# Kernel optimization log

Measured on AMD Instinct MI355X. Metric: run time of the kernel, lower is better.

## Reference

```python
import jax, jax.numpy as jnp
import numpy as np
from jax import lax

SPAN = 11
SIG_RGB = 0.1
SIG_XY = 6.0
SIG_DEPTH = 0.2


def _crf_energy(image, depth, yhat, m_dst, span=SPAN):
    """Vectorized equivalent of the 23x23 double loop.

    For offset d=(dx,dy), the torch code pairs t1 pixel u with t2 pixel u-d.
    jnp.roll(x, (dx,dy)) places x[u-d] at position u; a validity mask replaces
    the slicing.  Class-compatibility r = sum_{c1!=c2} p1[c1] p2[c2]
    = (sum p1)(sum p2) - <p1, p2>.
    """
    B, _, H, W = image.shape
    i = jnp.arange(H)
    j = jnp.arange(W)
    offs = np.array([(dx, dy) for dx in range(-span, span + 1) if dx != 0
                     for dy in range(-span, span + 1) if dy != 0], dtype=np.int32)
    offs = jnp.asarray(offs)  # (484, 2)
    s1 = yhat.sum(axis=1)  # (B,H,W), sums of softmax

    def body(carry, off):
        dx, dy = off[0], off[1]
        valid = (((i - dx >= 0) & (i - dx < H))[:, None]
                 & ((j - dy >= 0) & (j - dy < W))[None, :]).astype(image.dtype)  # (H,W)
        roll2 = lambda x: jnp.roll(x, (dx, dy), axis=(2, 3))
        r_img = roll2(image)
        r_yhat = roll2(yhat)
        r_depth = roll2(depth)
        r_dst = roll2(m_dst)
        drgb = (r_img - image) / SIG_RGB
        drgb_sq = (drgb * drgb).sum(axis=1)                       # (B,H,W)
        dind_sq = (dx * dx + dy * dy).astype(image.dtype) / (SIG_XY * SIG_XY)
        dd = (r_depth - depth) / SIG_DEPTH
        dd_sq = (dd * dd).sum(axis=1)                             # (B,H,W)
        kernel = jnp.exp(-0.5 * (drgb_sq + dind_sq)) + jnp.exp(-0.5 * dd_sq)
        m = r_dst[:, 0] * valid                                   # (B,H,W)
        compat = s1 * r_yhat.sum(axis=1) - (yhat * r_yhat).sum(axis=1)
        energy = (kernel * m * compat).sum() / m.sum()
        return carry, energy

    _, energies = lax.scan(body, None, offs)
    K = 2 * span + 1
    grid = jnp.zeros((K, K), dtype=image.dtype).at[offs[:, 0] + span, offs[:, 1] + span].set(energies)
    # result is (B, K, K) with the same scalar broadcast over batch -> mean == grid.mean()
    return grid.mean()


def setup_inputs() -> dict:
    key = jax.random.key(0)
    ks = jax.random.split(key, 6)
    B, C, H, W = 4, 3, 256, 512
    logit = jax.random.normal(ks[0], (B, C, H, W), dtype=jnp.float32)
    target = jax.random.randint(ks[1], (B, H, W), 0, C, dtype=jnp.int64)
    image = jax.random.uniform(ks[2], (B, 3, H, W), dtype=jnp.float32)
    depth = jax.random.uniform(ks[3], (B, 1, H, W), dtype=jnp.float32)
    destination_map = jax.random.uniform(ks[4], (B, 1, H, W), dtype=jnp.float32)
    source_map = jnp.ones((B, 1, H, W), dtype=jnp.float32)
    return {"logit": logit, "target": target, "image": image, "depth": depth,
            "destination_map": destination_map, "source_map": source_map}


def reference(logit, target, image, depth, destination_map, source_map):
    sg = lax.stop_gradient
    yhat = jax.nn.softmax(logit, axis=1)
    # compute_gcrf_new is called on .data (detached) tensors
    L_gcrf = _crf_energy(sg(image), sg(depth), sg(yhat), sg(destination_map))
    # CrossEntropyLoss(reduction='none')
    log_p = jax.nn.log_softmax(logit, axis=1)
    L_ce = -jnp.take_along_axis(log_p, target[:, None, :, :], axis=1)[:, 0]  # (B,H,W)
    dst = destination_map[:, 0]
    l1 = (L_ce * dst).mean()
    l2 = (L_ce * (1.0 - dst)).mean()
    count = sg(destination_map.mean())  # .item() in torch -> constant
    ce_loss = l1 * (1.0 - count) + l2 * count
    return ce_loss, L_gcrf
```

## Files before the change

### kernel.cpp

```cpp
#include <hip/hip_runtime.h>
#include <hip/hip_fp16.h>

#define H 256
#define W 512
#define HW (H*W)
#define NPIXF 524288.0f
#define SPAN 11
#define KK 23
#define NBINS (KK*KK)

#define LOG2E 1.4426950408889634f
#define CEXP  (-0.7213475204444817f)
#define CIND  (CEXP/36.0f)
#define KRGB  8.4932180f
#define KDEP  4.2466090f

#define TX 32
#define TYR 32
#define TROWS 43
#define TCOLS 43
#define TPIX (TROWS*TCOLS)

#define NTILE 512
#define NCRF (NTILE*2)
#define NSTAT 44

typedef _Float16 h2 __attribute__((ext_vector_type(2)));

struct alignas(16) PixV { h2 rg, bd, y01, y2m; };

__device__ __forceinline__ h2 pack2(float a, float b) {
  h2 r; r.x = (_Float16)a; r.y = (_Float16)b; return r;
}

__device__ __forceinline__ float dpp_sum(float x) {
  x += __int_as_float(__builtin_amdgcn_update_dpp(0, __float_as_int(x), 0x111, 0xf, 0xf, true));
  x += __int_as_float(__builtin_amdgcn_update_dpp(0, __float_as_int(x), 0x112, 0xf, 0xf, true));
  x += __int_as_float(__builtin_amdgcn_update_dpp(0, __float_as_int(x), 0x114, 0xf, 0xf, true));
  x += __int_as_float(__builtin_amdgcn_update_dpp(0, __float_as_int(x), 0x118, 0xf, 0xf, true));
  x += __int_as_float(__builtin_amdgcn_update_dpp(0, __float_as_int(x), 0x142, 0xa, 0xf, true));
  x += __int_as_float(__builtin_amdgcn_update_dpp(0, __float_as_int(x), 0x143, 0xc, 0xf, true));
  return x;
}

__device__ __forceinline__ float wave_sum(float x) {
  #pragma unroll
  for (int s = 1; s < 64; s <<= 1) x += __shfl_xor(x, s, 64);
  return x;
}

__device__ __forceinline__ float paircc(const PixV& C, const PixV& N,
                                        h2 nc01, h2 nc2z, float lind) {
  h2 drg = N.rg - C.rg;
  h2 dbd = N.bd - C.bd;
  h2 sq  = dbd*dbd;
  float dbsq = (float)sq.x;
  float ddsq = (float)sq.y;
#if __has_builtin(__builtin_amdgcn_fdot2)
  float q  = __builtin_amdgcn_fdot2(drg, drg, dbsq, false);
  float a1 = lind - q;
  float w1 = __builtin_amdgcn_fdot2(N.y01, nc01, 1.0f, false);
  float w  = __builtin_amdgcn_fdot2(N.y2m, nc2z, w1, false);
#else
  float dr = (float)drg.x, dg = (float)drg.y;
  float a1 = fmaf(-dr, dr, fmaf(-dg, dg, lind - dbsq));
  float ny0 = (float)N.y01.x, ny1 = (float)N.y01.y, ny2 = (float)N.y2m.x;
  float cy0 = (float)C.y01.x, cy1 = (float)C.y01.y, cy2 = (float)C.y2m.x;
  float w  = fmaf(-ny0, cy0, fmaf(-ny1, cy1, fmaf(-ny2, cy2, 1.0f)));
  (void)nc01; (void)nc2z;
#endif
  float kv = __builtin_amdgcn_exp2f(a1) + __builtin_amdgcn_exp2f(-ddsq);
  return kv * w;
}

__global__ __launch_bounds__(256, 4) void crf_kernel(
    const float* __restrict__ logit, const int* __restrict__ target,
    const float* __restrict__ image, const float* __restrict__ depth,
    const float* __restrict__ dst,
    float* __restrict__ g_bins, float* __restrict__ g_ce,
    float* __restrict__ rowBand, float* __restrict__ colBand) {
  __shared__ PixV  tile[TPIX];
  __shared__ float binsS[4][NBINS];
  __shared__ float redS[12];

  int tx = threadIdx.x;
  int bid = blockIdx.x;
  int lane = tx & 63;
  int wv = tx >> 6;

  if (bid >= NCRF) {
    int k = bid - NCRF;
    float s = 0.f;
    if (k < 22) {
      int row = (k < 11) ? k : (234 + k);
      for (int t = tx; t < 2048; t += 256) {
        int b = t >> 9, j = t & 511;
        s += dst[(size_t)b*HW + row*W + j];
      }
    } else {
      int kc = k - 22;
      int col = (kc < 11) ? kc : (490 + kc);
      for (int t = tx; t < 1024; t += 256) {
        int b = t >> 8, i = t & 255;
        s += dst[(size_t)b*HW + i*W + col];
      }
    }
    s = wave_sum(s);
    if (lane == 0) redS[wv] = s;
    __syncthreads();
    if (tx == 0) {
      float tot = redS[0] + redS[1] + redS[2] + redS[3];
      if (k < 22) rowBand[k] = tot; else colBand[k - 22] = tot;
    }
    return;
  }

  int tileId = bid >> 1;
  int half   = bid & 1;
  int bz = tileId >> 7;
  int rem = tileId & 127;
  int i0 = (rem >> 4) * TYR;
  int j0 = (rem & 15) * TX;
  int co = half ? 0 : 11;
  int cbase = j0 - co;

  const float* lg0 = logit + (size_t)bz*3*HW;
  const float* lg1 = lg0 + HW;
  const float* lg2 = lg0 + 2*HW;
  const float* im0 = image + (size_t)bz*3*HW;
  const float* im1 = im0 + HW;
  const float* im2 = im0 + 2*HW;
  const float* dep = depth + (size_t)bz*HW;
  const float* dsb = dst   + (size_t)bz*HW;
  const int*   tgb = target + (size_t)bz*HW;

  for (int s = tx; s < 4*NBINS; s += 256) ((float*)binsS)[s] = 0.f;

  float v0 = 0.f, v1 = 0.f, v2 = 0.f;
  for (int s = tx; s < TPIX; s += 256) {
    int r = s / TCOLS, c = s - r*TCOLS;
    int gi = i0 + r, gj = cbase + c;
    PixV ph;
    if (gi < H && (unsigned)gj < (unsigned)W) {
      int q = gi*W + gj;
      float l0 = lg0[q], l1 = lg1[q], l2 = lg2[q];
      float mx = fmaxf(l0, fmaxf(l1, l2));
      float e0 = __builtin_amdgcn_exp2f((l0-mx)*LOG2E);
      float e1 = __builtin_amdgcn_exp2f((l1-mx)*LOG2E);
      float e2 = __builtin_amdgcn_exp2f((l2-mx)*LOG2E);
      float S = e0+e1+e2;
      float inv = 1.0f/S;
      float m = dsb[q];
      ph.rg  = pack2(im0[q]*KRGB, im1[q]*KRGB);
      ph.bd  = pack2(im2[q]*KRGB, dep[q]*KDEP);
      ph.y01 = pack2(e0*inv, e1*inv);
      ph.y2m = pack2(e2*inv, m);
      if (half == 0 && r < TYR && c >= co && c < co+TX) {
        int t = tgb[q];
        float lt = (t==0) ? l0 : ((t==1) ? l1 : l2);
        float lce = mx + __logf(S) - lt;
        float t0 = lce * m;
        v0 += t0;
        v1 += lce - t0;
        v2 += m;
      }
    } else {
      ph.rg = ph.bd = pack2(1e30f, 1e30f);
      ph.y01 = ph.y2m = pack2(0.f, 0.f);
    }
    tile[s] = ph;
  }
  __syncthreads();

  int txc = tx & 31, ty = tx >> 5;
  int crow = ty*4;
  int cidx = crow*TCOLS + txc + co;
  PixV c0 = tile[cidx];
  PixV c1 = tile[cidx +   TCOLS];
  PixV c2 = tile[cidx + 2*TCOLS];
  PixV c3 = tile[cidx + 3*TCOLS];
  h2 nc01_0 = -c0.y01, nc01_1 = -c1.y01, nc01_2 = -c2.y01, nc01_3 = -c3.y01;
  h2 nc2z_0; nc2z_0.x = -c0.y2m.x; nc2z_0.y = (_Float16)0.f;
  h2 nc2z_1; nc2z_1.x = -c1.y2m.x; nc2z_1.y = (_Float16)0.f;
  h2 nc2z_2; nc2z_2.x = -c2.y2m.x; nc2z_2.y = (_Float16)0.f;
  h2 nc2z_3; nc2z_3.x = -c3.y2m.x; nc2z_3.y = (_Float16)0.f;
  float cm0 = (float)c0.y2m.y;
  float cm1 = (float)c1.y2m.y;
  float cm2 = (float)c2.y2m.y;
  float cm3 = (float)c3.y2m.y;

  int biLo = half * 11;
  #pragma unroll 1
  for (int bi = biLo; bi < biLo + 11; ++bi) {
    int db = bi - ((bi < 11) ? 11 : 10);
    int nb = cidx + db;
    float lb = CIND * (float)(db*db);
    int bb = SPAN*KK + (db + SPAN);
    PixV w0 = tile[nb +   TCOLS];
    PixV w1 = tile[nb + 2*TCOLS];
    PixV w2 = tile[nb + 3*TCOLS];
    float m0 = (float)w0.y2m.y;
    float m1 = (float)w1.y2m.y;
    float m2 = (float)w2.y2m.y;
    #pragma unroll
    for (int a = 1; a <= 11; ++a) {
      PixV w3 = tile[nb + (a+3)*TCOLS];
      float m3 = (float)w3.y2m.y;
      float lind = fmaf((float)(a*a), CIND, lb);
      float cc0 = paircc(c0, w0, nc01_0, nc2z_0, lind);
      float cc1 = paircc(c1, w1, nc01_1, nc2z_1, lind);
      float cc2 = paircc(c2, w2, nc01_2, nc2z_2, lind);
      float cc3 = paircc(c3, w3, nc01_3, nc2z_3, lind);
      float nd = fmaf(cc3, cm3, fmaf(cc2, cm2, fmaf(cc1, cm1, cc0*cm0)));
      float nr = fmaf(cc3, m3,  fmaf(cc2, m2,  fmaf(cc1, m1,  cc0*m0)));
      nd = dpp_sum(nd);
      nr = dpp_sum(nr);
      if (lane == 63) {
        int id = bb + a*KK;
        binsS[wv][id]       = nd;
        binsS[wv][528 - id] = nr;
      }
      w0 = w1; w1 = w2; w2 = w3;
      m0 = m1; m1 = m2; m2 = m3;
    }
  }
  __syncthreads();

  for (int s = tx; s < NBINS; s += 256) {
    float v = (binsS[0][s] + binsS[1][s]) + (binsS[2][s] + binsS[3][s]);
    if (v != 0.f) unsafeAtomicAdd(&g_bins[s], v);
  }
  if (half == 0) {
    v0 = dpp_sum(v0); v1 = dpp_sum(v1); v2 = dpp_sum(v2);
    if (lane == 63) { redS[wv] = v0; redS[4+wv] = v1; redS[8+wv] = v2; }
    __syncthreads();
    if (tx == 0) {
      unsafeAtomicAdd(&g_ce[0], redS[0]+redS[1]+redS[2]+redS[3]);
      unsafeAtomicAdd(&g_ce[1], redS[4]+redS[5]+redS[6]+redS[7]);
      unsafeAtomicAdd(&g_ce[2], redS[8]+redS[9]+redS[10]+redS[11]);
    }
  }
}

__global__ __launch_bounds__(256) void fin_kernel(const float* __restrict__ g_bins,
                                                  const float* __restrict__ g_ce,
                                                  const float* __restrict__ rowBand,
                                                  const float* __restrict__ colBand,
                                                  const float* __restrict__ dst,
                                                  float* __restrict__ out) {
  __shared__ float corner[22][22];
  __shared__ float rowp[22][23];
  __shared__ float P[23][23];
  __shared__ float rb[22], cb[22];
  __shared__ float TopP[12], BotS[12], LeftP[12], RightS[12];
  __shared__ float red[4];
  int tx = threadIdx.x;
  if (tx < 22) { rb[tx] = rowBand[tx]; cb[tx] = colBand[tx]; }
  for (int t = tx; t < 484; t += 256) {
    int ri = t / 22, ci = t - ri*22;
    int row = (ri < 11) ? ri : (234 + ri);
    int col = (ci < 11) ? ci : (490 + ci);
    float s = 0.f;
    #pragma unroll
    for (int b = 0; b < 4; ++b) s += dst[(size_t)b*HW + row*W + col];
    corner[ri][ci] = s;
  }
  __syncthreads();

  if (tx < 22) {
    float p = 0.f; rowp[tx][0] = 0.f;
    for (int j = 0; j < 22; ++j) { p += corner[tx][j]; rowp[tx][j+1] = p; }
  }
  else if (tx == 32) { float p=0.f; TopP[0]=0.f;   for (int k=1;k<12;++k){ p += rb[k-1];  TopP[k]=p; } }
  else if (tx == 33) { float p=0.f; BotS[0]=0.f;   for (int k=1;k<12;++k){ p += rb[22-k]; BotS[k]=p; } }
  else if (tx == 34) { float p=0.f; LeftP[0]=0.f;  for (int k=1;k<12;++k){ p += cb[k-1];  LeftP[k]=p; } }
  else if (tx == 35) { float p=0.f; RightS[0]=0.f; for (int k=1;k<12;++k){ p += cb[22-k]; RightS[k]=p; } }
  __syncthreads();

  if (tx < 23) {
    float p = 0.f; P[0][tx] = 0.f;
    for (int i = 0; i < 22; ++i) { p += rowp[i][tx]; P[i+1][tx] = p; }
  }
  __syncthreads();

  float S = g_ce[2];
  float esum = 0.f;
  for (int od = tx; od < NBINS; od += 256) {
    int dxp = od / KK, dyp = od - dxp*KK;
    int dx = dxp - SPAN, dy = dyp - SPAN;
    if (dx != 0 && dy != 0) {
      int ax = (dx < 0) ? -dx : 0;
      int bx = (dx > 0) ?  dx : 0;
      int ay = (dy < 0) ? -dy : 0;
      int by = (dy > 0) ?  dy : 0;
      float TLv = P[ax][ay];
      float TRv = P[ax][22] - P[ax][22-by];
      float BLv = P[22][ay] - P[22-bx][ay];
      float BRv = P[22][22] - P[22-bx][22] - P[22][22-by] + P[22-bx][22-by];
      float den = S - TopP[ax] - BotS[bx] - LeftP[ay] - RightS[by]
                + TLv + TRv + BLv + BRv;
      esum += g_bins[od] / den;
    }
  }
  esum = wave_sum(esum);
  int lane = tx & 63, wv = tx >> 6;
  if (lane == 0) red[wv] = esum;
  __syncthreads();
  if (tx == 0) {
    float E = (red[0]+red[1]+red[2]+red[3]) / 529.0f;
    float count = S / NPIXF;
    float l1 = g_ce[0] / NPIXF;
    float l2 = g_ce[1] / NPIXF;
    out[0] = l1*(1.0f - count) + l2*count;
    out[1] = E;
  }
}

extern "C" void kernel_launch(void* const* d_in, const int* in_sizes, int n_in,
                              void* d_out, int out_size, void* d_ws, size_t ws_size,
                              hipStream_t stream) {
  const float* logit  = (const float*)d_in[0];
  const int*   target = (const int*)  d_in[1];
  const float* image  = (const float*)d_in[2];
  const float* depth  = (const float*)d_in[3];
  const float* dstm   = (const float*)d_in[4];
  float* out = (float*)d_out;

  float* ws      = (float*)d_ws;
  float* g_bins  = ws;
  float* g_ce    = ws + NBINS;
  float* rowBand = ws + 532;
  float* colBand = ws + 554;

  hipMemsetAsync(ws, 0, 532*sizeof(float), stream);
  crf_kernel<<<NCRF + NSTAT, 256, 0, stream>>>(logit, target, image, depth, dstm,
                                               g_bins, g_ce, rowBand, colBand);
  fin_kernel<<<1, 256, 0, stream>>>(g_bins, g_ce, rowBand, colBand, dstm, out);
}
```

Before: 174.1 us.

## Pack row pairs into fp16x2 lanes and split pair loop by offset parity

Changes the shared tile layout so each 16-byte entry holds two vertically adjacent pixels, each channel stored as a packed fp16 pair. The pair-energy math, including exp2, then runs on packed half2 vectors. The grid is split four ways per tile, by column half and by parity of the row offset, so each block handles even or odd vertical offsets. The aim is to roughly halve the ALU and exp instruction count per pair and to raise block count. The cost is more duplicated tile loading and softmax work across blocks, plus lower precision in the exponent and weight math, now done fully in fp16.

```diff
diff --git a/kernel.cpp b/kernel.cpp
--- a/kernel.cpp
+++ b/kernel.cpp
@@ -19,18 +19,43 @@
 #define TYR 32
 #define TROWS 43
 #define TCOLS 43
-#define TPIX (TROWS*TCOLS)
+#define NP 22
 
 #define NTILE 512
-#define NCRF (NTILE*2)
+#define NCRF (NTILE*4)
 #define NSTAT 44
 
 typedef _Float16 h2 __attribute__((ext_vector_type(2)));
 
-struct alignas(16) PixV { h2 rg, bd, y01, y2m; };
+struct alignas(16) Pk1 { h2 rr, gg, bb, dd; };
+struct alignas(16) Pk2 { h2 y0, y1, y2, mm; };
 
 __device__ __forceinline__ h2 pack2(float a, float b) {
   h2 r; r.x = (_Float16)a; r.y = (_Float16)b; return r;
+}
+
+__device__ __forceinline__ h2 exp2pk(h2 x) {
+  __half2 hx = __builtin_bit_cast(__half2, x);
+  __half2 hr = h2exp2(hx);
+  return __builtin_bit_cast(h2, hr);
+}
+
+__device__ __forceinline__ h2 alignh(h2 a, h2 b) { h2 r; r.x = a.y; r.y = b.x; return r; }
+__device__ __forceinline__ Pk1 alignP1(const Pk1& a, const Pk1& b) {
+  Pk1 r; r.rr = alignh(a.rr,b.rr); r.gg = alignh(a.gg,b.gg);
+  r.bb = alignh(a.bb,b.bb); r.dd = alignh(a.dd,b.dd); return r;
+}
+__device__ __forceinline__ Pk2 alignP2(const Pk2& a, const Pk2& b) {
+  Pk2 r; r.y0 = alignh(a.y0,b.y0); r.y1 = alignh(a.y1,b.y1);
+  r.y2 = alignh(a.y2,b.y2); r.mm = alignh(a.mm,b.mm); return r;
+}
+
+__device__ __forceinline__ float fdot2f(h2 a, h2 b, float c) {
+#if __has_builtin(__builtin_amdgcn_fdot2)
+  return __builtin_amdgcn_fdot2(a, b, c, false);
+#else
+  return c + (float)a.x*(float)b.x + (float)a.y*(float)b.y;
+#endif
 }
 
 __device__ __forceinline__ float dpp_sum(float x) {
@@ -49,28 +74,76 @@
   return x;
 }
 
-__device__ __forceinline__ float paircc(const PixV& C, const PixV& N,
-                                        h2 nc01, h2 nc2z, float lind) {
-  h2 drg = N.rg - C.rg;
-  h2 dbd = N.bd - C.bd;
-  h2 sq  = dbd*dbd;
-  float dbsq = (float)sq.x;
-  float ddsq = (float)sq.y;
-#if __has_builtin(__builtin_amdgcn_fdot2)
-  float q  = __builtin_amdgcn_fdot2(drg, drg, dbsq, false);
-  float a1 = lind - q;
-  float w1 = __builtin_amdgcn_fdot2(N.y01, nc01, 1.0f, false);
-  float w  = __builtin_amdgcn_fdot2(N.y2m, nc2z, w1, false);
-#else
-  float dr = (float)drg.x, dg = (float)drg.y;
-  float a1 = fmaf(-dr, dr, fmaf(-dg, dg, lind - dbsq));
-  float ny0 = (float)N.y01.x, ny1 = (float)N.y01.y, ny2 = (float)N.y2m.x;
-  float cy0 = (float)C.y01.x, cy1 = (float)C.y01.y, cy2 = (float)C.y2m.x;
-  float w  = fmaf(-ny0, cy0, fmaf(-ny1, cy1, fmaf(-ny2, cy2, 1.0f)));
-  (void)nc01; (void)nc2z;
-#endif
-  float kv = __builtin_amdgcn_exp2f(a1) + __builtin_amdgcn_exp2f(-ddsq);
+__device__ __forceinline__ h2 ccpk(const Pk1& C1, const Pk2& C2,
+                                   const Pk1& W1, const Pk2& W2, h2 lpk) {
+  h2 dr  = W1.rr - C1.rr;
+  h2 dg  = W1.gg - C1.gg;
+  h2 dbv = W1.bb - C1.bb;
+  h2 dd  = W1.dd - C1.dd;
+  h2 rs  = dr*dr + dg*dg + dbv*dbv;
+  h2 a1  = lpk - rs;
+  h2 a2  = -(dd*dd);
+  h2 kv  = exp2pk(a1) + exp2pk(a2);
+  h2 one; one.x = (_Float16)1.f; one.y = (_Float16)1.f;
+  h2 w   = one - W2.y0*C2.y0 - W2.y1*C2.y1 - W2.y2*C2.y2;
   return kv * w;
+}
+
+template<int APAR>
+__device__ __forceinline__ void pairLoop(const Pk1* t1, const Pk2* t2,
+                                         float (*binsS)[NBINS], int tx, int half) {
+  int lane = tx & 63, wv = tx >> 6;
+  int txc = tx & 31, ty = tx >> 5;
+  int crow = ty*4;
+  int q0 = crow >> 1;
+  int co = half ? 0 : 11;
+  int ccol = txc + co;
+
+  Pk1 cA1, cB1; Pk2 cA2, cB2;
+  if (APAR == 0) {
+    cA1 = t1[q0*TCOLS + ccol];      cA2 = t2[q0*TCOLS + ccol];
+    cB1 = t1[(q0+1)*TCOLS + ccol];  cB2 = t2[(q0+1)*TCOLS + ccol];
+  } else {
+    Pk1 pa = t1[q0*TCOLS+ccol], pb = t1[(q0+1)*TCOLS+ccol], pc = t1[(q0+2)*TCOLS+ccol];
+    Pk2 qa = t2[q0*TCOLS+ccol], qb = t2[(q0+1)*TCOLS+ccol], qc = t2[(q0+2)*TCOLS+ccol];
+    cA1 = alignP1(pa, pb); cB1 = alignP1(pb, pc);
+    cA2 = alignP2(qa, qb); cB2 = alignP2(qb, qc);
+  }
+
+  int biLo = half * 11;
+  #pragma unroll 1
+  for (int bi = biLo; bi < biLo + 11; ++bi) {
+    int db = bi - ((bi < 11) ? 11 : 10);
+    int nbcol = ccol + db;
+    float lb = CIND * (float)(db*db);
+    int bb = SPAN*KK + (db + SPAN);
+    int qw = q0 + 1;
+    Pk1 wA1 = t1[qw*TCOLS + nbcol];      Pk2 wA2 = t2[qw*TCOLS + nbcol];
+    Pk1 wB1 = t1[(qw+1)*TCOLS + nbcol];  Pk2 wB2 = t2[(qw+1)*TCOLS + nbcol];
+    constexpr int NS = APAR ? 6 : 5;
+    #pragma unroll
+    for (int s = 0; s < NS; ++s) {
+      if (s > 0) {
+        wA1 = wB1; wA2 = wB2;
+        wB1 = t1[(qw+s+1)*TCOLS + nbcol]; wB2 = t2[(qw+s+1)*TCOLS + nbcol];
+      }
+      int a = APAR ? (2*s+1) : (2*s+2);
+      float lind = fmaf((float)(a*a), CIND, lb);
+      h2 lpk = pack2(lind, lind);
+      h2 ccA = ccpk(cA1, cA2, wA1, wA2, lpk);
+      h2 ccB = ccpk(cB1, cB2, wB1, wB2, lpk);
+      float nd = fdot2f(ccA, cA2.mm, 0.f);
+      nd = fdot2f(ccB, cB2.mm, nd);
+      float nr = fdot2f(ccA, wA2.mm, 0.f);
+      nr = fdot2f(ccB, wB2.mm, nr);
+      nd = dpp_sum(nd); nr = dpp_sum(nr);
+      if (lane == 63) {
+        int id = bb + a*KK;
+        binsS[wv][id]       = nd;
+        binsS[wv][528 - id] = nr;
+      }
+    }
+  }
 }
 
 __global__ __launch_bounds__(256, 4) void crf_kernel(
@@ -79,7 +152,8 @@
     const float* __restrict__ dst,
     float* __restrict__ g_bins, float* __restrict__ g_ce,
     float* __restrict__ rowBand, float* __restrict__ colBand) {
-  __shared__ PixV  tile[TPIX];
+  __shared__ Pk1 t1[NP*TCOLS];
+  __shared__ Pk2 t2[NP*TCOLS];
   __shared__ float binsS[4][NBINS];
   __shared__ float redS[12];
 
@@ -115,14 +189,17 @@
     return;
   }
 
-  int tileId = bid >> 1;
-  int half   = bid & 1;
+  int tileId = bid >> 2;
+  int sub    = bid & 3;
+  int half   = sub >> 1;
+  int apar   = sub & 1;
   int bz = tileId >> 7;
   int rem = tileId & 127;
   int i0 = (rem >> 4) * TYR;
   int j0 = (rem & 15) * TX;
   int co = half ? 0 : 11;
   int cbase = j0 - co;
+  bool ceB = (half == 0) && (apar == 0);
 
   const float* lg0 = logit + (size_t)bz*3*HW;
   const float* lg1 = lg0 + HW;
@@ -137,100 +214,59 @@
   for (int s = tx; s < 4*NBINS; s += 256) ((float*)binsS)[s] = 0.f;
 
   float v0 = 0.f, v1 = 0.f, v2 = 0.f;
-  for (int s = tx; s < TPIX; s += 256) {
-    int r = s / TCOLS, c = s - r*TCOLS;
-    int gi = i0 + r, gj = cbase + c;
-    PixV ph;
-    if (gi < H && (unsigned)gj < (unsigned)W) {
-      int q = gi*W + gj;
-      float l0 = lg0[q], l1 = lg1[q], l2 = lg2[q];
-      float mx = fmaxf(l0, fmaxf(l1, l2));
-      float e0 = __builtin_amdgcn_exp2f((l0-mx)*LOG2E);
-      float e1 = __builtin_amdgcn_exp2f((l1-mx)*LOG2E);
-      float e2 = __builtin_amdgcn_exp2f((l2-mx)*LOG2E);
-      float S = e0+e1+e2;
-      float inv = 1.0f/S;
-      float m = dsb[q];
-      ph.rg  = pack2(im0[q]*KRGB, im1[q]*KRGB);
-      ph.bd  = pack2(im2[q]*KRGB, dep[q]*KDEP);
-      ph.y01 = pack2(e0*inv, e1*inv);
-      ph.y2m = pack2(e2*inv, m);
-      if (half == 0 && r < TYR && c >= co && c < co+TX) {
-        int t = tgb[q];
-        float lt = (t==0) ? l0 : ((t==1) ? l1 : l2);
-        float lce = mx + __logf(S) - lt;
-        float t0 = lce * m;
-        v0 += t0;
-        v1 += lce - t0;
-        v2 += m;
-      }
-    } else {
-      ph.rg = ph.bd = pack2(1e30f, 1e30f);
-      ph.y01 = ph.y2m = pack2(0.f, 0.f);
-    }
-    tile[s] = ph;
-  }
-  __syncthreads();
-
-  int txc = tx & 31, ty = tx >> 5;
-  int crow = ty*4;
-  int cidx = crow*TCOLS + txc + co;
-  PixV c0 = tile[cidx];
-  PixV c1 = tile[cidx +   TCOLS];
-  PixV c2 = tile[cidx + 2*TCOLS];
-  PixV c3 = tile[cidx + 3*TCOLS];
-  h2 nc01_0 = -c0.y01, nc01_1 = -c1.y01, nc01_2 = -c2.y01, nc01_3 = -c3.y01;
-  h2 nc2z_0; nc2z_0.x = -c0.y2m.x; nc2z_0.y = (_Float16)0.f;
-  h2 nc2z_1; nc2z_1.x = -c1.y2m.x; nc2z_1.y = (_Float16)0.f;
-  h2 nc2z_2; nc2z_2.x = -c2.y2m.x; nc2z_2.y = (_Float16)0.f;
-  h2 nc2z_3; nc2z_3.x = -c3.y2m.x; nc2z_3.y = (_Float16)0.f;
-  float cm0 = (float)c0.y2m.y;
-  float cm1 = (float)c1.y2m.y;
-  float cm2 = (float)c2.y2m.y;
-  float cm3 = (float)c3.y2m.y;
-
-  int biLo = half * 11;
-  #pragma unroll 1
-  for (int bi = biLo; bi < biLo + 11; ++bi) {
-    int db = bi - ((bi < 11) ? 11 : 10);
-    int nb = cidx + db;
-    float lb = CIND * (float)(db*db);
-    int bb = SPAN*KK + (db + SPAN);
-    PixV w0 = tile[nb +   TCOLS];
-    PixV w1 = tile[nb + 2*TCOLS];
-    PixV w2 = tile[nb + 3*TCOLS];
-    float m0 = (float)w0.y2m.y;
-    float m1 = (float)w1.y2m.y;
-    float m2 = (float)w2.y2m.y;
+  for (int s = tx; s < NP*TCOLS; s += 256) {
+    int q = s / TCOLS, c = s - q*TCOLS;
+    int gj = cbase + c;
+    float fr[2], fg[2], fb[2], fd[2], f0[2], f1[2], f2[2], fm[2];
     #pragma unroll
-    for (int a = 1; a <= 11; ++a) {
-      PixV w3 = tile[nb + (a+3)*TCOLS];
-      float m3 = (float)w3.y2m.y;
-      float lind = fmaf((float)(a*a), CIND, lb);
-      float cc0 = paircc(c0, w0, nc01_0, nc2z_0, lind);
-      float cc1 = paircc(c1, w1, nc01_1, nc2z_1, lind);
-      float cc2 = paircc(c2, w2, nc01_2, nc2z_2, lind);
-      float cc3 = paircc(c3, w3, nc01_3, nc2z_3, lind);
-      float nd = fmaf(cc3, cm3, fmaf(cc2, cm2, fmaf(cc1, cm1, cc0*cm0)));
-      float nr = fmaf(cc3, m3,  fmaf(cc2, m2,  fmaf(cc1, m1,  cc0*m0)));
-      nd = dpp_sum(nd);
-      nr = dpp_sum(nr);
-      if (lane == 63) {
-        int id = bb + a*KK;
-        binsS[wv][id]       = nd;
-        binsS[wv][528 - id] = nr;
-      }
-      w0 = w1; w1 = w2; w2 = w3;
-      m0 = m1; m1 = m2; m2 = m3;
-    }
-  }
+    for (int hh = 0; hh < 2; ++hh) {
+      int r = 2*q - apar + hh;
+      int gi = i0 + r;
+      bool ok = (r >= 0) && (r < TROWS) && (gi < H) && ((unsigned)gj < (unsigned)W);
+      if (ok) {
+        int qq = gi*W + gj;
+        float l0 = lg0[qq], l1 = lg1[qq], l2 = lg2[qq];
+        float mx = fmaxf(l0, fmaxf(l1, l2));
+        float e0 = __builtin_amdgcn_exp2f((l0-mx)*LOG2E);
+        float e1 = __builtin_amdgcn_exp2f((l1-mx)*LOG2E);
+        float e2 = __builtin_amdgcn_exp2f((l2-mx)*LOG2E);
+        float S = e0+e1+e2;
+        float inv = 1.0f/S;
+        float m = dsb[qq];
+        fr[hh] = im0[qq]*KRGB; fg[hh] = im1[qq]*KRGB;
+        fb[hh] = im2[qq]*KRGB; fd[hh] = dep[qq]*KDEP;
+        f0[hh] = e0*inv; f1[hh] = e1*inv; f2[hh] = e2*inv; fm[hh] = m;
+        if (ceB && r < TYR && c >= co && c < co+TX) {
+          int t = tgb[qq];
+          float lt = (t==0) ? l0 : ((t==1) ? l1 : l2);
+          float lce = mx + __logf(S) - lt;
+          float t0 = lce * m;
+          v0 += t0;
+          v1 += lce - t0;
+          v2 += m;
+        }
+      } else {
+        fr[hh] = fg[hh] = fb[hh] = fd[hh] = 1e30f;
+        f0[hh] = f1[hh] = f2[hh] = fm[hh] = 0.f;
+      }
+    }
+    Pk1 p1; p1.rr = pack2(fr[0],fr[1]); p1.gg = pack2(fg[0],fg[1]);
+            p1.bb = pack2(fb[0],fb[1]); p1.dd = pack2(fd[0],fd[1]);
+    Pk2 p2; p2.y0 = pack2(f0[0],f0[1]); p2.y1 = pack2(f1[0],f1[1]);
+            p2.y2 = pack2(f2[0],f2[1]); p2.mm = pack2(fm[0],fm[1]);
+    t1[s] = p1; t2[s] = p2;
+  }
+  __syncthreads();
+
+  if (apar == 0) pairLoop<0>(t1, t2, binsS, tx, half);
+  else           pairLoop<1>(t1, t2, binsS, tx, half);
   __syncthreads();
 
   for (int s = tx; s < NBINS; s += 256) {
     float v = (binsS[0][s] + binsS[1][s]) + (binsS[2][s] + binsS[3][s]);
     if (v != 0.f) unsafeAtomicAdd(&g_bins[s], v);
   }
-  if (half == 0) {
+  if (ceB) {
     v0 = dpp_sum(v0); v1 = dpp_sum(v1); v2 = dpp_sum(v2);
     if (lane == 63) { redS[wv] = v0; redS[4+wv] = v1; redS[8+wv] = v2; }
     __syncthreads();
```

After: 164.0 us. -5.8%, faster.
